# Optimization experiments

Hardware: AMD Instinct MI355X
Metric: run time of the kernel (lower is better)

The kernel has to match this reference:

```python
import jax, jax.numpy as jnp
import numpy as np

# ---- static radial-bin geometry (h == w == 512) ----
H = W = 512
_y, _x = np.indices((H, W))
_center = np.array([(_x.max() - _x.min()) / 2.0, (_y.max() - _y.min()) / 2.0])
_r = np.hypot(_x - _center[0], _y - _center[1])
_r_int = _r.astype(int)
NBINS = int(_r_int.max()) + 1            # all integer radii 0..NBINS-1 are present
R_INT = jnp.asarray(_r_int.ravel())       # (H*W,) int32 bin id per pixel
COUNTS = jnp.asarray(np.bincount(_r_int.ravel(), minlength=NBINS).astype(np.float32))

EPS = 1e-8


def _get_mask(freq_ri):
    """Vectorized equivalent of PSDLoss.get_mask. freq_ri: (n,c,h,w,2).

    azimuthalAverage's sort+cumsum binning == per-integer-radius mean,
    excluding bin 0 and the last bin. The sequential np.where idx-scan in
    psd1D_circle_mask is equivalent to a gather psd_ext[r_int] because psd
    values lie in [0,1] (the only possible collision, value 1.0 at idx=1,
    rewrites bin 0 with psd_ext[1] == psd_ext[0], a no-op).
    """
    comp = (freq_ri[..., 0] + EPS) + 1j * freq_ri[..., 1]   # freq_np += 1e-8
    mag = 20.0 * jnp.log(jnp.abs(comp))                      # magnitude spectrum
    n, c, h, w = mag.shape
    flat = mag.reshape(n, c, h * w)
    seg = lambda m: jax.ops.segment_sum(m, R_INT, num_segments=NBINS)
    sums = jax.vmap(jax.vmap(seg))(flat)                     # (n,c,NBINS)
    binmean = sums / COUNTS
    psd = binmean[..., 1:NBINS - 1]                          # bins 1..NBINS-2
    pmin = psd.min(axis=-1, keepdims=True)
    pmax = psd.max(axis=-1, keepdims=True)
    psd = (psd - pmin) / (pmax - pmin)                       # normalize to [0,1]
    # extend: prepend psd[0], append 0 -> length NBINS, indexed by r_int
    zero = jnp.zeros(psd.shape[:-1] + (1,), psd.dtype)
    psd_ext = jnp.concatenate([psd[..., :1], psd, zero], axis=-1)  # (n,c,NBINS)
    mask = jnp.take(psd_ext, R_INT, axis=-1).reshape(n, c, h, w)
    return mask


def _tensor2freq(img):
    f = jnp.fft.fftshift(jnp.fft.fft2(img), axes=(2, 3))
    return jnp.stack([f.real, f.imag], axis=-1)              # (n,c,h,w,2)


def reference(pred, target):
    loss_weight = 1.0
    pred_freq = _tensor2freq(pred)
    target_freq = _tensor2freq(target)
    # norm='l2', weight='recon', matrix=None (defaults)
    tmp = pred_freq ** 2 - target_freq ** 2
    tmp = tmp[..., 0] + tmp[..., 1]
    freq_distance = tmp ** 2
    mask_all = jax.lax.stop_gradient(_get_mask(pred_freq))   # detached weight
    wmat = 1.0 - mask_all
    wmat = jnp.where(jnp.isnan(wmat), 0.0, wmat)
    wmat = jnp.clip(wmat, 0.0, 1.0)
    return jnp.mean(wmat * freq_distance) * loss_weight


def setup_inputs() -> dict:
    key = jax.random.key(0)
    k1, k2 = jax.random.split(key)
    pred = jax.random.normal(k1, (8, 3, 512, 512), dtype=jnp.float32)
    target = jax.random.normal(k2, (8, 3, 512, 512), dtype=jnp.float32)
    return {"pred": pred, "target": target}
```

## Files before the change

### kernel.cpp

```cpp
#include <hip/hip_runtime.h>
#include <math.h>

#define HW 512
#define NIMG 24
#define NB 362
#define PLANE (HW*HW)
#define NC 257
#define NG 65
#define NPB (NIMG*NG)
#define CP2 133120

#define OFF_PM  0
#define OFF_PD  (NPB*NB)
#define OFF_PR  (2*NPB*NB)
#define OFF_PIm (OFF_PR + NIMG*CP2)
#define OFF_TR  (OFF_PR + 2*NIMG*CP2)
#define OFF_TI  (OFF_PR + 3*NIMG*CP2)
#define OFF_RM  (OFF_PR + 4*NIMG*CP2)
#define OFF_RD  (OFF_RM + NIMG*NB)

__device__ __forceinline__ int rbin_odd(float u, float v) {
    return (int)(sqrtf(fmaf(u, u, v*v)) * 0.5f);
}

__device__ __forceinline__ void cmul(float& xr, float& xi, float wr, float wi) {
    float r = xr*wr - xi*wi;
    xi = xr*wi + xi*wr;
    xr = r;
}

__device__ __forceinline__ void dft8(float ar[8], float ai[8]) {
    const float C = 0.70710678118654752440f;
    float t0r=ar[0]+ar[4], t0i=ai[0]+ai[4];
    float t1r=ar[0]-ar[4], t1i=ai[0]-ai[4];
    float t2r=ar[2]+ar[6], t2i=ai[2]+ai[6];
    float t3r=ar[2]-ar[6], t3i=ai[2]-ai[6];
    float E0r=t0r+t2r, E0i=t0i+t2i;
    float E2r=t0r-t2r, E2i=t0i-t2i;
    float E1r=t1r+t3i, E1i=t1i-t3r;
    float E3r=t1r-t3i, E3i=t1i+t3r;
    float u0r=ar[1]+ar[5], u0i=ai[1]+ai[5];
    float u1r=ar[1]-ar[5], u1i=ai[1]-ai[5];
    float u2r=ar[3]+ar[7], u2i=ai[3]+ai[7];
    float u3r=ar[3]-ar[7], u3i=ai[3]-ai[7];
    float O0r=u0r+u2r, O0i=u0i+u2i;
    float O2r=u0r-u2r, O2i=u0i-u2i;
    float O1r=u1r+u3i, O1i=u1i-u3r;
    float O3r=u1r-u3i, O3i=u1i+u3r;
    float W1r = C*(O1r+O1i), W1i = C*(O1i-O1r);
    float W2r = O2i,         W2i = -O2r;
    float W3r = C*(O3i-O3r), W3i = -C*(O3r+O3i);
    ar[0]=E0r+O0r; ai[0]=E0i+O0i;
    ar[4]=E0r-O0r; ai[4]=E0i-O0i;
    ar[1]=E1r+W1r; ai[1]=E1i+W1i;
    ar[5]=E1r-W1r; ai[5]=E1i-W1i;
    ar[2]=E2r+W2r; ai[2]=E2i+W2i;
    ar[6]=E2r-W2r; ai[6]=E2i-W2i;
    ar[3]=E3r+W3r; ai[3]=E3i+W3i;
    ar[7]=E3r-W3r; ai[7]=E3i-W3i;
}

__device__ __forceinline__ void twiddle7(float ar[8], float ai[8], float wr, float wi) {
    float pr = wr, pi = wi;
    cmul(ar[1], ai[1], pr, pi);
    #pragma unroll
    for (int k = 2; k < 8; ++k) {
        float nr = pr*wr - pi*wi;
        pi = pr*wi + pi*wr;
        pr = nr;
        cmul(ar[k], ai[k], pr, pi);
    }
}

__device__ __forceinline__ void fft512x2(float Ar[8], float Ai[8],
                                         float Br[8], float Bi[8],
                                         float* Lr, float* Li, int lane) {
    float s1, c1, s2, c2;
    int k1 = lane >> 3, b = lane & 7;
    __sincosf((float)lane * (-6.28318530717958647692f/512.0f), &s1, &c1);
    __sincosf((float)b    * (-6.28318530717958647692f/64.0f),  &s2, &c2);
    dft8(Ar, Ai); twiddle7(Ar, Ai, c1, s1);
    dft8(Br, Bi); twiddle7(Br, Bi, c1, s1);
    #pragma unroll
    for (int j = 0; j < 8; ++j) { Lr[j*68+lane] = Ar[j]; Li[j*68+lane] = Ai[j]; }
    #pragma unroll
    for (int a = 0; a < 8; ++a) { Ar[a] = Lr[k1*68+8*a+b]; Ai[a] = Li[k1*68+8*a+b]; }
    #pragma unroll
    for (int j = 0; j < 8; ++j) { Lr[j*68+lane] = Br[j]; Li[j*68+lane] = Bi[j]; }
    dft8(Ar, Ai); twiddle7(Ar, Ai, c2, s2);
    #pragma unroll
    for (int a = 0; a < 8; ++a) { Br[a] = Lr[k1*68+8*a+b]; Bi[a] = Li[k1*68+8*a+b]; }
    dft8(Br, Bi); twiddle7(Br, Bi, c2, s2);
    #pragma unroll
    for (int cc = 0; cc < 8; ++cc) {
        int ad = k1*68 + 8*cc + ((b + cc) & 7);
        Lr[ad] = Ar[cc]; Li[ad] = Ai[cc];
    }
    #pragma unroll
    for (int bb = 0; bb < 8; ++bb) {
        int ad = k1*68 + 8*b + ((bb + b) & 7);
        Ar[bb] = Lr[ad]; Ai[bb] = Li[ad];
    }
    #pragma unroll
    for (int cc = 0; cc < 8; ++cc) {
        int ad = k1*68 + 8*cc + ((b + cc) & 7);
        Lr[ad] = Br[cc]; Li[ad] = Bi[cc];
    }
    dft8(Ar, Ai);
    #pragma unroll
    for (int bb = 0; bb < 8; ++bb) {
        int ad = k1*68 + 8*b + ((bb + b) & 7);
        Br[bb] = Lr[ad]; Bi[bb] = Li[ad];
    }
    dft8(Br, Bi);
}

__global__ __launch_bounds__(256, 4) void k_rowfft(const float* __restrict__ pred,
                                                   const float* __restrict__ tgt,
                                                   float* __restrict__ ws) {
    __shared__ float smem[4352];
    int t = threadIdx.x, lane = t & 63, w = t >> 6;
    int b = blockIdx.x;
    int img = b >> 6;
    int r0 = (b & 63) << 3;
    int rA = r0 + 2*w;
    const float* pA = pred + (size_t)img*PLANE + (size_t)rA*HW;
    const float* tA = tgt  + (size_t)img*PLANE + (size_t)rA*HW;
    float arA[8], aiA[8], arB[8], aiB[8];
    #pragma unroll
    for (int j = 0; j < 8; ++j) {
        arA[j] = pA[64*j + lane];      aiA[j] = tA[64*j + lane];
        arB[j] = pA[HW + 64*j + lane]; aiB[j] = tA[HW + 64*j + lane];
    }
    float* Lr = smem + w*1088;
    float* Li = Lr + 544;
    fft512x2(arA, aiA, arB, aiB, Lr, Li, lane);
    float PrA[4], PiA[4], TrA[4], TiA[4], P256A=0.f, T256A=0.f;
    float PrB[4], PiB[4], TrB[4], TiB[4], P256B=0.f, T256B=0.f;
    #pragma unroll
    for (int d = 0; d < 8; ++d) {
        int k = (lane>>3) + ((lane&7)<<3) + (d<<6);
        Lr[k] = arA[d]; Li[k] = aiA[d];
    }
    #pragma unroll
    for (int m = 0; m < 4; ++m) {
        int kk = 64*m + lane, j2 = (512 - kk) & 511;
        float z1r = Lr[kk], z1i = Li[kk], z2r = Lr[j2], z2i = Li[j2];
        PrA[m] = 0.5f*(z1r+z2r); PiA[m] = 0.5f*(z1i-z2i);
        TrA[m] = 0.5f*(z1i+z2i); TiA[m] = 0.5f*(z2r-z1r);
    }
    if (lane == 0) { P256A = Lr[256]; T256A = Li[256]; }
    #pragma unroll
    for (int d = 0; d < 8; ++d) {
        int k = (lane>>3) + ((lane&7)<<3) + (d<<6);
        Lr[k] = arB[d]; Li[k] = aiB[d];
    }
    #pragma unroll
    for (int m = 0; m < 4; ++m) {
        int kk = 64*m + lane, j2 = (512 - kk) & 511;
        float z1r = Lr[kk], z1i = Li[kk], z2r = Lr[j2], z2i = Li[j2];
        PrB[m] = 0.5f*(z1r+z2r); PiB[m] = 0.5f*(z1i-z2i);
        TrB[m] = 0.5f*(z1i+z2i); TiB[m] = 0.5f*(z2r-z1r);
    }
    if (lane == 0) { P256B = Lr[256]; T256B = Li[256]; }

    float* tR = smem;
    float* tI = smem + 2080;
    __syncthreads();
    #pragma unroll
    for (int m = 0; m < 4; ++m) {
        int kk = 64*m + lane;
        tR[(2*w)*260 + kk]   = PrA[m]; tR[(2*w+1)*260 + kk] = PrB[m];
        tI[(2*w)*260 + kk]   = PiA[m]; tI[(2*w+1)*260 + kk] = PiB[m];
    }
    if (lane == 0) {
        tR[(2*w)*260 + 256] = P256A; tR[(2*w+1)*260 + 256] = P256B;
        tI[(2*w)*260 + 256] = 0.f;   tI[(2*w+1)*260 + 256] = 0.f;
    }
    __syncthreads();
    for (int idx = t; idx < 1040; idx += 256) {
        int comp = idx >= 520;
        int q = idx - (comp ? 520 : 0);
        int cg = q >> 3, rl = q & 7;
        const float* Tt = comp ? tI : tR;
        float4 v = *(const float4*)(Tt + rl*260 + 4*cg);
        float* outP = ws + (size_t)(comp ? OFF_PIm : OFF_PR)
                      + (size_t)img*CP2 + cg*2048 + (r0 + rl)*4;
        *(float4*)outP = v;
    }
    __syncthreads();
    #pragma unroll
    for (int m = 0; m < 4; ++m) {
        int kk = 64*m + lane;
        tR[(2*w)*260 + kk]   = TrA[m]; tR[(2*w+1)*260 + kk] = TrB[m];
        tI[(2*w)*260 + kk]   = TiA[m]; tI[(2*w+1)*260 + kk] = TiB[m];
    }
    if (lane == 0) {
        tR[(2*w)*260 + 256] = T256A; tR[(2*w+1)*260 + 256] = T256B;
        tI[(2*w)*260 + 256] = 0.f;   tI[(2*w+1)*260 + 256] = 0.f;
    }
    __syncthreads();
    for (int idx = t; idx < 1040; idx += 256) {
        int comp = idx >= 520;
        int q = idx - (comp ? 520 : 0);
        int cg = q >> 3, rl = q & 7;
        const float* Tt = comp ? tI : tR;
        float4 v = *(const float4*)(Tt + rl*260 + 4*cg);
        float* outP = ws + (size_t)(comp ? OFF_TI : OFF_TR)
                      + (size_t)img*CP2 + cg*2048 + (r0 + rl)*4;
        *(float4*)outP = v;
    }
}

__device__ __forceinline__ void flush2(float* binM, float* binD, int k,
                                       float aM, float aD) {
    atomicAdd(&binM[k], aM);
    atomicAdd(&binD[k], aD);
}

__global__ __launch_bounds__(256, 4) void k_colfft(const float* __restrict__ ws,
                                                   float* __restrict__ gPM,
                                                   float* __restrict__ gPD) {
    __shared__ float smem[4352];
    __shared__ float binM[NB], binD[NB];
    int t = threadIdx.x, lane = t & 63, w = t >> 6;
    for (int j = t; j < NB; j += 256) { binM[j] = 0.f; binD[j] = 0.f; }
    __syncthreads();
    int b = blockIdx.x;
    int img = b / NG;
    int g = b - img*NG;
    int c = 4*g + w;
    if (c < NC) {
        float* Lr = smem + w*1088;
        float* Li = Lr + 544;
        float prm[8], pim[8], trm[8], tim[8];
        size_t cbase = (size_t)img*CP2 + (size_t)(c >> 2)*2048 + (c & 3);
        const float* cPR = ws + OFF_PR  + cbase;
        const float* cPI = ws + OFF_PIm + cbase;
        const float* cTR = ws + OFF_TR  + cbase;
        const float* cTI = ws + OFF_TI  + cbase;
        #pragma unroll
        for (int j = 0; j < 8; ++j) {
            int o = (64*j + lane) << 2;
            prm[j] = cPR[o]; pim[j] = cPI[o];
            trm[j] = cTR[o]; tim[j] = cTI[o];
        }
        fft512x2(prm, pim, trm, tim, Lr, Li, lane);
        #pragma unroll
        for (int d = 0; d < 8; ++d) {
            int ky = (lane>>3) + ((lane&7)<<3) + (d<<6);
            float sp  = prm[d]*prm[d] + pim[d]*pim[d];
            float st_ = trm[d]*trm[d] + tim[d]*tim[d];
            float diff = sp - st_;
            float er = prm[d] + 1e-8f;
            Lr[ky] = 10.0f * __logf(er*er + pim[d]*pim[d]);
            Li[ky] = diff*diff;
        }
        __builtin_amdgcn_wave_barrier();
        int p0 = 4*lane;
        float4 fM = *(const float4*)(Lr + p0);
        float4 fD = *(const float4*)(Li + p0);
        float4 bM = *(const float4*)(Lr + 508 - p0);
        float4 bD = *(const float4*)(Li + 508 - p0);
        float eM = Lr[p0 + 4], eD = Li[p0 + 4];
        int gidx = (512 - p0) & 511;
        float gM = Lr[gidx], gD = Li[gidx];
        float sM[4], sD[4];
        sM[0]=fM.x+bM.w; sM[1]=fM.y+bM.z; sM[2]=fM.z+bM.y; sM[3]=fM.w+bM.x;
        sD[0]=fD.x+bD.w; sD[1]=fD.y+bD.z; sD[2]=fD.z+bD.y; sD[3]=fD.w+bD.x;
        float v1 = (c == 256) ? 511.0f : (float)(2*c + 1);
        {
            int kp = rbin_odd((float)(2*p0 + 1), v1);
            float aM = sM[0], aD = sD[0];
            #pragma unroll
            for (int j = 1; j < 4; ++j) {
                int k = rbin_odd((float)(2*(p0 + j) + 1), v1);
                if (k == kp) { aM += sM[j]; aD += sD[j]; }
                else { flush2(binM, binD, kp, aM, aD); kp = k; aM = sM[j]; aD = sD[j]; }
            }
            flush2(binM, binD, kp, aM, aD);
        }
        if (c >= 1 && c <= 255) {
            float s2M[4], s2D[4];
            s2M[0]=gM+fM.y;   s2D[0]=gD+fD.y;
            s2M[1]=bM.w+fM.z; s2D[1]=bD.w+fD.z;
            s2M[2]=bM.z+fM.w; s2D[2]=bD.z+fD.w;
            s2M[3]=bM.y+eM;   s2D[3]=bD.y+eD;
            float v2 = (float)(2*c - 1);
            int kp = rbin_odd((float)(2*p0 + 1), v2);
            float aM = s2M[0], aD = s2D[0];
            #pragma unroll
            for (int j = 1; j < 4; ++j) {
                int k = rbin_odd((float)(2*(p0 + j) + 1), v2);
                if (k == kp) { aM += s2M[j]; aD += s2D[j]; }
                else { flush2(binM, binD, kp, aM, aD); kp = k; aM = s2M[j]; aD = s2D[j]; }
            }
            flush2(binM, binD, kp, aM, aD);
        }
    }
    __syncthreads();
    for (int j = t; j < NB; j += 256) {
        gPM[(size_t)b*NB + j] = binM[j];
        gPD[(size_t)b*NB + j] = binD[j];
    }
}

__global__ __launch_bounds__(256) void k_reduce(const float* __restrict__ gPM,
                                                const float* __restrict__ gPD,
                                                float* __restrict__ rM,
                                                float* __restrict__ rD) {
    __shared__ float sm[8][33], sd2[8][33];
    int b = blockIdx.x;
    int img = b / 12, ch = b - img*12;
    int jl = threadIdx.x & 31, gs = threadIdx.x >> 5;
    int j = ch*32 + jl;
    float aM = 0.f, aD = 0.f;
    if (j < NB) {
        for (int g = gs; g < NG; g += 8) {
            aM += gPM[(size_t)(img*NG + g)*NB + j];
            aD += gPD[(size_t)(img*NG + g)*NB + j];
        }
    }
    sm[gs][jl] = aM; sd2[gs][jl] = aD;
    __syncthreads();
    if (threadIdx.x < 32 && j < NB) {
        float tM = 0.f, tD = 0.f;
        #pragma unroll
        for (int s = 0; s < 8; ++s) { tM += sm[s][jl]; tD += sd2[s][jl]; }
        rM[img*NB + j] = tM;
        rD[img*NB + j] = tD;
    }
}

__global__ __launch_bounds__(512) void k_final(const float* __restrict__ rM,
                                               const float* __restrict__ rD,
                                               float* __restrict__ out) {
    __shared__ int cnt[NB];
    __shared__ float meanb[NB];
    __shared__ float dsum[NB];
    __shared__ float rmin[512], rmax[512];
    __shared__ double sred[512];
    int t = threadIdx.x, img = blockIdx.x;
    for (int j = t; j < NB; j += 512) cnt[j] = 0;
    __syncthreads();
    {
        float u = (float)(2*(t >> 1) + 1);
        int vb = (t & 1) << 7;
        int kp = rbin_odd(u, (float)(2*vb + 1));
        int acc = 4;
        for (int i = 1; i < 128; ++i) {
            int k = rbin_odd(u, (float)(2*(vb + i) + 1));
            if (k == kp) acc += 4;
            else { atomicAdd(&cnt[kp], acc); kp = k; acc = 4; }
        }
        atomicAdd(&cnt[kp], acc);
    }
    __syncthreads();
    for (int j = t; j < NB; j += 512) {
        meanb[j] = rM[img*NB + j] / (float)cnt[j];
        dsum[j]  = rD[img*NB + j];
    }
    __syncthreads();
    float vmin = INFINITY, vmax = -INFINITY;
    if (t >= 1 && t <= 360) { vmin = meanb[t]; vmax = meanb[t]; }
    rmin[t] = vmin; rmax[t] = vmax;
    __syncthreads();
    for (int s = 256; s > 0; s >>= 1) {
        if (t < s) {
            float a = rmin[t], bb = rmin[t+s];
            rmin[t] = (a != a || bb != bb) ? __int_as_float(0x7fc00000) : fminf(a, bb);
            a = rmax[t]; bb = rmax[t+s];
            rmax[t] = (a != a || bb != bb) ? __int_as_float(0x7fc00000) : fmaxf(a, bb);
        }
        __syncthreads();
    }
    float pmin = rmin[0], pmax = rmax[0];
    double part = 0.0;
    for (int k = t; k < NB; k += 512) {
        float wgt;
        if (k == NB - 1) {
            wgt = 1.0f;
        } else {
            int idx = (k == 0) ? 1 : k;
            float e = (meanb[idx] - pmin) / (pmax - pmin);
            float wv = 1.0f - e;
            if (wv != wv) wv = 0.0f;
            wv = fminf(fmaxf(wv, 0.0f), 1.0f);
            wgt = wv;
        }
        part += (double)wgt * (double)dsum[k];
    }
    sred[t] = part;
    __syncthreads();
    for (int s = 256; s > 0; s >>= 1) {
        if (t < s) sred[t] += sred[t+s];
        __syncthreads();
    }
    if (t == 0) atomicAdd(out, (float)(sred[0] / 6291456.0));
}

extern "C" void kernel_launch(void* const* d_in, const int* in_sizes, int n_in,
                              void* d_out, int out_size, void* d_ws, size_t ws_size,
                              hipStream_t stream) {
    const float* pred = (const float*)d_in[0];
    const float* tgt  = (const float*)d_in[1];
    float* ws = (float*)d_ws;
    hipMemsetAsync(d_out, 0, sizeof(float), stream);
    k_rowfft<<<NIMG*64, 256, 0, stream>>>(pred, tgt, ws);
    k_colfft<<<NPB, 256, 0, stream>>>(ws, ws + OFF_PM, ws + OFF_PD);
    k_reduce<<<NIMG*12, 256, 0, stream>>>(ws + OFF_PM, ws + OFF_PD,
                                          ws + OFF_RM, ws + OFF_RD);
    k_final<<<NIMG, 512, 0, stream>>>(ws + OFF_RM, ws + OFF_RD, (float*)d_out);
}
```

Baseline: 155.8 us.

## Reorder row-FFT intermediate layout so column FFT loads contiguous float4 pairs

Each row-FFT block now handles rows strided by 64 (qb, qb+64, ...) instead of 8 consecutive rows, and writes its per-column results as 8 contiguous floats at col*512 + qb*8. That places the elements each column-FFT lane needs, rows lane+64*j, next to each other, so the column kernel reads them with two float4 loads per array instead of eight strided scalar loads. The intermediate buffer shrinks to 257*512 per image. In exchange, the shared-memory transpose reads become scalar and strided, and the global writes are 32-byte chunks spread across columns.

```diff
diff --git a/kernel.cpp b/kernel.cpp
--- a/kernel.cpp
+++ b/kernel.cpp
@@ -8,15 +8,16 @@
 #define NC 257
 #define NG 65
 #define NPB (NIMG*NG)
-#define CP2 133120
+#define CPC 131584
+
 
 #define OFF_PM  0
 #define OFF_PD  (NPB*NB)
 #define OFF_PR  (2*NPB*NB)
-#define OFF_PIm (OFF_PR + NIMG*CP2)
-#define OFF_TR  (OFF_PR + 2*NIMG*CP2)
-#define OFF_TI  (OFF_PR + 3*NIMG*CP2)
-#define OFF_RM  (OFF_PR + 4*NIMG*CP2)
+#define OFF_PIm (OFF_PR + NIMG*CPC)
+#define OFF_TR  (OFF_PR + 2*NIMG*CPC)
+#define OFF_TI  (OFF_PR + 3*NIMG*CPC)
+#define OFF_RM  (OFF_PR + 4*NIMG*CPC)
 #define OFF_RD  (OFF_RM + NIMG*NB)
 
 __device__ __forceinline__ int rbin_odd(float u, float v) {
@@ -122,15 +123,15 @@
     int t = threadIdx.x, lane = t & 63, w = t >> 6;
     int b = blockIdx.x;
     int img = b >> 6;
-    int r0 = (b & 63) << 3;
-    int rA = r0 + 2*w;
+    int qb = b & 63;
+    int rA = 128*w + qb;
     const float* pA = pred + (size_t)img*PLANE + (size_t)rA*HW;
     const float* tA = tgt  + (size_t)img*PLANE + (size_t)rA*HW;
     float arA[8], aiA[8], arB[8], aiB[8];
     #pragma unroll
     for (int j = 0; j < 8; ++j) {
-        arA[j] = pA[64*j + lane];      aiA[j] = tA[64*j + lane];
-        arB[j] = pA[HW + 64*j + lane]; aiB[j] = tA[HW + 64*j + lane];
+        arA[j] = pA[64*j + lane];         aiA[j] = tA[64*j + lane];
+        arB[j] = pA[64*HW + 64*j + lane]; aiB[j] = tA[64*HW + 64*j + lane];
     }
     float* Lr = smem + w*1088;
     float* Li = Lr + 544;
@@ -178,15 +179,19 @@
         tI[(2*w)*260 + 256] = 0.f;   tI[(2*w+1)*260 + 256] = 0.f;
     }
     __syncthreads();
-    for (int idx = t; idx < 1040; idx += 256) {
-        int comp = idx >= 520;
-        int q = idx - (comp ? 520 : 0);
-        int cg = q >> 3, rl = q & 7;
+    for (int idx = t; idx < 514; idx += 256) {
+        int comp = idx >= 257;
+        int col = comp ? (idx - 257) : idx;
         const float* Tt = comp ? tI : tR;
-        float4 v = *(const float4*)(Tt + rl*260 + 4*cg);
+        float4 v0, v1;
+        v0.x = Tt[        col]; v0.y = Tt[ 260 + col];
+        v0.z = Tt[ 520 + col];  v0.w = Tt[ 780 + col];
+        v1.x = Tt[1040 + col];  v1.y = Tt[1300 + col];
+        v1.z = Tt[1560 + col];  v1.w = Tt[1820 + col];
         float* outP = ws + (size_t)(comp ? OFF_PIm : OFF_PR)
-                      + (size_t)img*CP2 + cg*2048 + (r0 + rl)*4;
-        *(float4*)outP = v;
+                      + (size_t)img*CPC + (size_t)col*512 + qb*8;
+        *(float4*)outP = v0;
+        *(float4*)(outP + 4) = v1;
     }
     __syncthreads();
     #pragma unroll
@@ -200,15 +205,19 @@
         tI[(2*w)*260 + 256] = 0.f;   tI[(2*w+1)*260 + 256] = 0.f;
     }
     __syncthreads();
-    for (int idx = t; idx < 1040; idx += 256) {
-        int comp = idx >= 520;
-        int q = idx - (comp ? 520 : 0);
-        int cg = q >> 3, rl = q & 7;
+    for (int idx = t; idx < 514; idx += 256) {
+        int comp = idx >= 257;
+        int col = comp ? (idx - 257) : idx;
         const float* Tt = comp ? tI : tR;
-        float4 v = *(const float4*)(Tt + rl*260 + 4*cg);
+        float4 v0, v1;
+        v0.x = Tt[        col]; v0.y = Tt[ 260 + col];
+        v0.z = Tt[ 520 + col];  v0.w = Tt[ 780 + col];
+        v1.x = Tt[1040 + col];  v1.y = Tt[1300 + col];
+        v1.z = Tt[1560 + col];  v1.w = Tt[1820 + col];
         float* outP = ws + (size_t)(comp ? OFF_TI : OFF_TR)
-                      + (size_t)img*CP2 + cg*2048 + (r0 + rl)*4;
-        *(float4*)outP = v;
+                      + (size_t)img*CPC + (size_t)col*512 + qb*8;
+        *(float4*)outP = v0;
+        *(float4*)(outP + 4) = v1;
     }
 }
 
@@ -233,18 +242,19 @@
     if (c < NC) {
         float* Lr = smem + w*1088;
         float* Li = Lr + 544;
-        float prm[8], pim[8], trm[8], tim[8];
-        size_t cbase = (size_t)img*CP2 + (size_t)(c >> 2)*2048 + (c & 3);
-        const float* cPR = ws + OFF_PR  + cbase;
-        const float* cPI = ws + OFF_PIm + cbase;
-        const float* cTR = ws + OFF_TR  + cbase;
-        const float* cTI = ws + OFF_TI  + cbase;
-        #pragma unroll
-        for (int j = 0; j < 8; ++j) {
-            int o = (64*j + lane) << 2;
-            prm[j] = cPR[o]; pim[j] = cPI[o];
-            trm[j] = cTR[o]; tim[j] = cTI[o];
-        }
+        size_t cb = (size_t)img*CPC + (size_t)c*512 + (size_t)(lane*8);
+        const float* cPR = ws + OFF_PR  + cb;
+        const float* cPI = ws + OFF_PIm + cb;
+        const float* cTR = ws + OFF_TR  + cb;
+        const float* cTI = ws + OFF_TI  + cb;
+        float4 pr0 = *(const float4*)cPR, pr1 = *(const float4*)(cPR + 4);
+        float4 pi0 = *(const float4*)cPI, pi1 = *(const float4*)(cPI + 4);
+        float4 tr0 = *(const float4*)cTR, tr1 = *(const float4*)(cTR + 4);
+        float4 ti0 = *(const float4*)cTI, ti1 = *(const float4*)(cTI + 4);
+        float prm[8] = {pr0.x,pr0.y,pr0.z,pr0.w,pr1.x,pr1.y,pr1.z,pr1.w};
+        float pim[8] = {pi0.x,pi0.y,pi0.z,pi0.w,pi1.x,pi1.y,pi1.z,pi1.w};
+        float trm[8] = {tr0.x,tr0.y,tr0.z,tr0.w,tr1.x,tr1.y,tr1.z,tr1.w};
+        float tim[8] = {ti0.x,ti0.y,ti0.z,ti0.w,ti1.x,ti1.y,ti1.z,ti1.w};
         fft512x2(prm, pim, trm, tim, Lr, Li, lane);
         #pragma unroll
         for (int d = 0; d < 8; ++d) {
```

New measurement: 167.8 us. 7.7% more time.

## Process two columns per wave in column FFT and halve block count

Applied to the files above, without the earlier changes.

The column-FFT kernel now has each wave transform two complex columns at once (four real signals: pred and target for each), using a new four-way FFT that interleaves the two columns' radix-8 stages through float2 shared memory. The grid shrinks to about half as many blocks, which halves the per-block partial bin arrays and the work in the reduce kernel. This aims to raise instruction-level parallelism per wave and cut block overhead and partial-sum traffic. In exchange it doubles register pressure per thread under launch_bounds(256,4), which can cause spills or lower occupancy, and the shared-memory footprint doubles.

```diff
diff --git a/kernel.cpp b/kernel.cpp
--- a/kernel.cpp
+++ b/kernel.cpp
@@ -6,13 +6,13 @@
 #define NB 362
 #define PLANE (HW*HW)
 #define NC 257
-#define NG 65
-#define NPB (NIMG*NG)
+#define NG2 33
+#define NPB2 (NIMG*NG2)
 #define CP2 133120
 
 #define OFF_PM  0
-#define OFF_PD  (NPB*NB)
-#define OFF_PR  (2*NPB*NB)
+#define OFF_PD  (NPB2*NB)
+#define OFF_PR  (2*NPB2*NB)
 #define OFF_PIm (OFF_PR + NIMG*CP2)
 #define OFF_TR  (OFF_PR + 2*NIMG*CP2)
 #define OFF_TI  (OFF_PR + 3*NIMG*CP2)
@@ -115,6 +115,84 @@
     dft8(Br, Bi);
 }
 
+__device__ __forceinline__ void fft512x4(
+        float Ar[8], float Ai[8], float Br[8], float Bi[8],
+        float Cr[8], float Ci[8], float Dr[8], float Di[8],
+        float2* L1, float2* L2, int lane) {
+    float s1, c1, s2, c2;
+    int k1 = lane >> 3, b = lane & 7;
+    __sincosf((float)lane * (-6.28318530717958647692f/512.0f), &s1, &c1);
+    __sincosf((float)b    * (-6.28318530717958647692f/64.0f),  &s2, &c2);
+    dft8(Ar, Ai); twiddle7(Ar, Ai, c1, s1);
+    dft8(Br, Bi); twiddle7(Br, Bi, c1, s1);
+    dft8(Cr, Ci); twiddle7(Cr, Ci, c1, s1);
+    dft8(Dr, Di); twiddle7(Dr, Di, c1, s1);
+    #pragma unroll
+    for (int j = 0; j < 8; ++j) L1[j*68+lane] = make_float2(Ar[j], Ai[j]);
+    #pragma unroll
+    for (int j = 0; j < 8; ++j) L2[j*68+lane] = make_float2(Cr[j], Ci[j]);
+    #pragma unroll
+    for (int a = 0; a < 8; ++a) { float2 v = L1[k1*68+8*a+b]; Ar[a]=v.x; Ai[a]=v.y; }
+    #pragma unroll
+    for (int a = 0; a < 8; ++a) { float2 v = L2[k1*68+8*a+b]; Cr[a]=v.x; Ci[a]=v.y; }
+    #pragma unroll
+    for (int j = 0; j < 8; ++j) L1[j*68+lane] = make_float2(Br[j], Bi[j]);
+    #pragma unroll
+    for (int j = 0; j < 8; ++j) L2[j*68+lane] = make_float2(Dr[j], Di[j]);
+    dft8(Ar, Ai); twiddle7(Ar, Ai, c2, s2);
+    dft8(Cr, Ci); twiddle7(Cr, Ci, c2, s2);
+    #pragma unroll
+    for (int a = 0; a < 8; ++a) { float2 v = L1[k1*68+8*a+b]; Br[a]=v.x; Bi[a]=v.y; }
+    #pragma unroll
+    for (int a = 0; a < 8; ++a) { float2 v = L2[k1*68+8*a+b]; Dr[a]=v.x; Di[a]=v.y; }
+    dft8(Br, Bi); twiddle7(Br, Bi, c2, s2);
+    dft8(Dr, Di); twiddle7(Dr, Di, c2, s2);
+    #pragma unroll
+    for (int cc = 0; cc < 8; ++cc) {
+        int ad = k1*68 + 8*cc + ((b + cc) & 7);
+        L1[ad] = make_float2(Ar[cc], Ai[cc]);
+    }
+    #pragma unroll
+    for (int cc = 0; cc < 8; ++cc) {
+        int ad = k1*68 + 8*cc + ((b + cc) & 7);
+        L2[ad] = make_float2(Cr[cc], Ci[cc]);
+    }
+    #pragma unroll
+    for (int bb = 0; bb < 8; ++bb) {
+        int ad = k1*68 + 8*b + ((bb + b) & 7);
+        float2 v = L1[ad]; Ar[bb] = v.x; Ai[bb] = v.y;
+    }
+    #pragma unroll
+    for (int bb = 0; bb < 8; ++bb) {
+        int ad = k1*68 + 8*b + ((bb + b) & 7);
+        float2 v = L2[ad]; Cr[bb] = v.x; Ci[bb] = v.y;
+    }
+    #pragma unroll
+    for (int cc = 0; cc < 8; ++cc) {
+        int ad = k1*68 + 8*cc + ((b + cc) & 7);
+        L1[ad] = make_float2(Br[cc], Bi[cc]);
+    }
+    #pragma unroll
+    for (int cc = 0; cc < 8; ++cc) {
+        int ad = k1*68 + 8*cc + ((b + cc) & 7);
+        L2[ad] = make_float2(Dr[cc], Di[cc]);
+    }
+    dft8(Ar, Ai);
+    dft8(Cr, Ci);
+    #pragma unroll
+    for (int bb = 0; bb < 8; ++bb) {
+        int ad = k1*68 + 8*b + ((bb + b) & 7);
+        float2 v = L1[ad]; Br[bb] = v.x; Bi[bb] = v.y;
+    }
+    #pragma unroll
+    for (int bb = 0; bb < 8; ++bb) {
+        int ad = k1*68 + 8*b + ((bb + b) & 7);
+        float2 v = L2[ad]; Dr[bb] = v.x; Di[bb] = v.y;
+    }
+    dft8(Br, Bi);
+    dft8(Dr, Di);
+}
+
 __global__ __launch_bounds__(256, 4) void k_rowfft(const float* __restrict__ pred,
                                                    const float* __restrict__ tgt,
                                                    float* __restrict__ ws) {
@@ -218,85 +296,104 @@
     atomicAdd(&binD[k], aD);
 }
 
+__device__ __forceinline__ void bin_column(const float2* LC, int c, int lane,
+                                           float* binM, float* binD) {
+    int p0 = 4*lane;
+    float4 q0  = *(const float4*)(LC + p0);
+    float4 q1  = *(const float4*)(LC + p0 + 2);
+    float4 r0v = *(const float4*)(LC + (508 - p0));
+    float4 r1v = *(const float4*)(LC + (510 - p0));
+    float2 e2 = LC[p0 + 4];
+    float2 g2 = LC[(512 - p0) & 511];
+    float sM[4], sD[4];
+    sM[0]=q0.x+r1v.z; sM[1]=q0.z+r1v.x; sM[2]=q1.x+r0v.z; sM[3]=q1.z+r0v.x;
+    sD[0]=q0.y+r1v.w; sD[1]=q0.w+r1v.y; sD[2]=q1.y+r0v.w; sD[3]=q1.w+r0v.y;
+    float v1 = (c == 256) ? 511.0f : (float)(2*c + 1);
+    {
+        int kp = rbin_odd((float)(2*p0 + 1), v1);
+        float aM = sM[0], aD = sD[0];
+        #pragma unroll
+        for (int j = 1; j < 4; ++j) {
+            int k = rbin_odd((float)(2*(p0 + j) + 1), v1);
+            if (k == kp) { aM += sM[j]; aD += sD[j]; }
+            else { flush2(binM, binD, kp, aM, aD); kp = k; aM = sM[j]; aD = sD[j]; }
+        }
+        flush2(binM, binD, kp, aM, aD);
+    }
+    if (c >= 1 && c <= 255) {
+        float s2M[4], s2D[4];
+        s2M[0]=g2.x+q0.z;   s2D[0]=g2.y+q0.w;
+        s2M[1]=r1v.z+q1.x;  s2D[1]=r1v.w+q1.y;
+        s2M[2]=r1v.x+q1.z;  s2D[2]=r1v.y+q1.w;
+        s2M[3]=r0v.z+e2.x;  s2D[3]=r0v.w+e2.y;
+        float v2 = (float)(2*c - 1);
+        int kp = rbin_odd((float)(2*p0 + 1), v2);
+        float aM = s2M[0], aD = s2D[0];
+        #pragma unroll
+        for (int j = 1; j < 4; ++j) {
+            int k = rbin_odd((float)(2*(p0 + j) + 1), v2);
+            if (k == kp) { aM += s2M[j]; aD += s2D[j]; }
+            else { flush2(binM, binD, kp, aM, aD); kp = k; aM = s2M[j]; aD = s2D[j]; }
+        }
+        flush2(binM, binD, kp, aM, aD);
+    }
+}
+
 __global__ __launch_bounds__(256, 4) void k_colfft(const float* __restrict__ ws,
                                                    float* __restrict__ gPM,
                                                    float* __restrict__ gPD) {
-    __shared__ float smem[4352];
+    __shared__ __align__(16) float2 smem2[4352];
     __shared__ float binM[NB], binD[NB];
     int t = threadIdx.x, lane = t & 63, w = t >> 6;
     for (int j = t; j < NB; j += 256) { binM[j] = 0.f; binD[j] = 0.f; }
     __syncthreads();
     int b = blockIdx.x;
-    int img = b / NG;
-    int g = b - img*NG;
-    int c = 4*g + w;
-    if (c < NC) {
-        float* Lr = smem + w*1088;
-        float* Li = Lr + 544;
-        float prm[8], pim[8], trm[8], tim[8];
-        size_t cbase = (size_t)img*CP2 + (size_t)(c >> 2)*2048 + (c & 3);
-        const float* cPR = ws + OFF_PR  + cbase;
-        const float* cPI = ws + OFF_PIm + cbase;
-        const float* cTR = ws + OFF_TR  + cbase;
-        const float* cTI = ws + OFF_TI  + cbase;
+    int img = b / NG2;
+    int g = b - img*NG2;
+    int cA = 8*g + w;
+    int cB = cA + 4;
+    bool doA = (cA < NC), doB = (cB < NC);
+    if (doA) {
+        float2* L1 = smem2 + w*1088;
+        float2* L2 = L1 + 544;
+        float pr1[8], pi1[8], tr1[8], ti1[8];
+        float pr2[8], pi2[8], tr2[8], ti2[8];
+        size_t cbA = (size_t)img*CP2 + (size_t)(cA >> 2)*2048 + (cA & 3);
+        size_t cbB = doB ? (cbA + 2048) : cbA;
+        const float* aPR = ws + OFF_PR  + cbA;
+        const float* aPI = ws + OFF_PIm + cbA;
+        const float* aTR = ws + OFF_TR  + cbA;
+        const float* aTI = ws + OFF_TI  + cbA;
+        const float* bPR = ws + OFF_PR  + cbB;
+        const float* bPI = ws + OFF_PIm + cbB;
+        const float* bTR = ws + OFF_TR  + cbB;
+        const float* bTI = ws + OFF_TI  + cbB;
         #pragma unroll
         for (int j = 0; j < 8; ++j) {
             int o = (64*j + lane) << 2;
-            prm[j] = cPR[o]; pim[j] = cPI[o];
-            trm[j] = cTR[o]; tim[j] = cTI[o];
-        }
-        fft512x2(prm, pim, trm, tim, Lr, Li, lane);
+            pr1[j] = aPR[o]; pi1[j] = aPI[o];
+            tr1[j] = aTR[o]; ti1[j] = aTI[o];
+            pr2[j] = bPR[o]; pi2[j] = bPI[o];
+            tr2[j] = bTR[o]; ti2[j] = bTI[o];
+        }
+        fft512x4(pr1, pi1, tr1, ti1, pr2, pi2, tr2, ti2, L1, L2, lane);
         #pragma unroll
         for (int d = 0; d < 8; ++d) {
             int ky = (lane>>3) + ((lane&7)<<3) + (d<<6);
-            float sp  = prm[d]*prm[d] + pim[d]*pim[d];
-            float st_ = trm[d]*trm[d] + tim[d]*tim[d];
-            float diff = sp - st_;
-            float er = prm[d] + 1e-8f;
-            Lr[ky] = 10.0f * __logf(er*er + pim[d]*pim[d]);
-            Li[ky] = diff*diff;
+            float spA = pr1[d]*pr1[d] + pi1[d]*pi1[d];
+            float stA = tr1[d]*tr1[d] + ti1[d]*ti1[d];
+            float dfA = spA - stA;
+            float erA = pr1[d] + 1e-8f;
+            L1[ky] = make_float2(10.0f * __logf(erA*erA + pi1[d]*pi1[d]), dfA*dfA);
+            float spB = pr2[d]*pr2[d] + pi2[d]*pi2[d];
+            float stB = tr2[d]*tr2[d] + ti2[d]*ti2[d];
+            float dfB = spB - stB;
+            float erB = pr2[d] + 1e-8f;
+            L2[ky] = make_float2(10.0f * __logf(erB*erB + pi2[d]*pi2[d]), dfB*dfB);
         }
         __builtin_amdgcn_wave_barrier();
-        int p0 = 4*lane;
-        float4 fM = *(const float4*)(Lr + p0);
-        float4 fD = *(const float4*)(Li + p0);
-        float4 bM = *(const float4*)(Lr + 508 - p0);
-        float4 bD = *(const float4*)(Li + 508 - p0);
-        float eM = Lr[p0 + 4], eD = Li[p0 + 4];
-        int gidx = (512 - p0) & 511;
-        float gM = Lr[gidx], gD = Li[gidx];
-        float sM[4], sD[4];
-        sM[0]=fM.x+bM.w; sM[1]=fM.y+bM.z; sM[2]=fM.z+bM.y; sM[3]=fM.w+bM.x;
-        sD[0]=fD.x+bD.w; sD[1]=fD.y+bD.z; sD[2]=fD.z+bD.y; sD[3]=fD.w+bD.x;
-        float v1 = (c == 256) ? 511.0f : (float)(2*c + 1);
-        {
-            int kp = rbin_odd((float)(2*p0 + 1), v1);
-            float aM = sM[0], aD = sD[0];
-            #pragma unroll
-            for (int j = 1; j < 4; ++j) {
-                int k = rbin_odd((float)(2*(p0 + j) + 1), v1);
-                if (k == kp) { aM += sM[j]; aD += sD[j]; }
-                else { flush2(binM, binD, kp, aM, aD); kp = k; aM = sM[j]; aD = sD[j]; }
-            }
-            flush2(binM, binD, kp, aM, aD);
-        }
-        if (c >= 1 && c <= 255) {
-            float s2M[4], s2D[4];
-            s2M[0]=gM+fM.y;   s2D[0]=gD+fD.y;
-            s2M[1]=bM.w+fM.z; s2D[1]=bD.w+fD.z;
-            s2M[2]=bM.z+fM.w; s2D[2]=bD.z+fD.w;
-            s2M[3]=bM.y+eM;   s2D[3]=bD.y+eD;
-            float v2 = (float)(2*c - 1);
-            int kp = rbin_odd((float)(2*p0 + 1), v2);
-            float aM = s2M[0], aD = s2D[0];
-            #pragma unroll
-            for (int j = 1; j < 4; ++j) {
-                int k = rbin_odd((float)(2*(p0 + j) + 1), v2);
-                if (k == kp) { aM += s2M[j]; aD += s2D[j]; }
-                else { flush2(binM, binD, kp, aM, aD); kp = k; aM = s2M[j]; aD = s2D[j]; }
-            }
-            flush2(binM, binD, kp, aM, aD);
-        }
+        bin_column(L1, cA, lane, binM, binD);
+        if (doB) bin_column(L2, cB, lane, binM, binD);
     }
     __syncthreads();
     for (int j = t; j < NB; j += 256) {
@@ -316,9 +413,9 @@
     int j = ch*32 + jl;
     float aM = 0.f, aD = 0.f;
     if (j < NB) {
-        for (int g = gs; g < NG; g += 8) {
-            aM += gPM[(size_t)(img*NG + g)*NB + j];
-            aD += gPD[(size_t)(img*NG + g)*NB + j];
+        for (int g = gs; g < NG2; g += 8) {
+            aM += gPM[(size_t)(img*NG2 + g)*NB + j];
+            aD += gPD[(size_t)(img*NG2 + g)*NB + j];
         }
     }
     sm[gs][jl] = aM; sd2[gs][jl] = aD;
@@ -407,7 +504,7 @@
     float* ws = (float*)d_ws;
     hipMemsetAsync(d_out, 0, sizeof(float), stream);
     k_rowfft<<<NIMG*64, 256, 0, stream>>>(pred, tgt, ws);
-    k_colfft<<<NPB, 256, 0, stream>>>(ws, ws + OFF_PM, ws + OFF_PD);
+    k_colfft<<<NPB2, 256, 0, stream>>>(ws, ws + OFF_PM, ws + OFF_PD);
     k_reduce<<<NIMG*12, 256, 0, stream>>>(ws + OFF_PM, ws + OFF_PD,
                                           ws + OFF_RM, ws + OFF_RD);
     k_final<<<NIMG, 512, 0, stream>>>(ws + OFF_RM, ws + OFF_RD, (float*)d_out);
```

Measured after the change: 162.1 us. +4.0%, slower.

## Split column FFT of pred and target across separate waves per column

Applied to the files above, without the earlier changes.

The column-FFT kernel now uses 512 threads per block, so each column gets two waves: one transforms the pred spectrum and the other the target spectrum, each with a single-signal FFT in interleaved float2 LDS. The waves exchange magnitude and power results through shared memory after a block barrier. Binning also splits by role: one wave handles the primary mirror pairing and the other the secondary pairing. The aim is more parallelism and lower per-thread register pressure. The cost is a block-wide sync and more LDS traffic per column.

```diff
diff --git a/kernel.cpp b/kernel.cpp
--- a/kernel.cpp
+++ b/kernel.cpp
@@ -115,6 +115,31 @@
     dft8(Br, Bi);
 }
 
+__device__ __forceinline__ void fft512x1(float Ar[8], float Ai[8],
+                                         float2* L, int lane) {
+    float s1, c1, s2, c2;
+    int k1 = lane >> 3, b = lane & 7;
+    __sincosf((float)lane * (-6.28318530717958647692f/512.0f), &s1, &c1);
+    __sincosf((float)b    * (-6.28318530717958647692f/64.0f),  &s2, &c2);
+    dft8(Ar, Ai); twiddle7(Ar, Ai, c1, s1);
+    #pragma unroll
+    for (int j = 0; j < 8; ++j) L[j*68+lane] = make_float2(Ar[j], Ai[j]);
+    #pragma unroll
+    for (int a = 0; a < 8; ++a) { float2 v = L[k1*68+8*a+b]; Ar[a]=v.x; Ai[a]=v.y; }
+    dft8(Ar, Ai); twiddle7(Ar, Ai, c2, s2);
+    #pragma unroll
+    for (int cc = 0; cc < 8; ++cc) {
+        int ad = k1*68 + 8*cc + ((b + cc) & 7);
+        L[ad] = make_float2(Ar[cc], Ai[cc]);
+    }
+    #pragma unroll
+    for (int bb = 0; bb < 8; ++bb) {
+        int ad = k1*68 + 8*b + ((bb + b) & 7);
+        float2 v = L[ad]; Ar[bb] = v.x; Ai[bb] = v.y;
+    }
+    dft8(Ar, Ai);
+}
+
 __global__ __launch_bounds__(256, 4) void k_rowfft(const float* __restrict__ pred,
                                                    const float* __restrict__ tgt,
                                                    float* __restrict__ ws) {
@@ -218,58 +243,72 @@
     atomicAdd(&binD[k], aD);
 }
 
-__global__ __launch_bounds__(256, 4) void k_colfft(const float* __restrict__ ws,
+__global__ __launch_bounds__(512, 4) void k_colfft(const float* __restrict__ ws,
                                                    float* __restrict__ gPM,
                                                    float* __restrict__ gPD) {
-    __shared__ float smem[4352];
+    __shared__ __align__(16) float2 scr[8*544];
     __shared__ float binM[NB], binD[NB];
     int t = threadIdx.x, lane = t & 63, w = t >> 6;
-    for (int j = t; j < NB; j += 256) { binM[j] = 0.f; binD[j] = 0.f; }
+    for (int j = t; j < NB; j += 512) { binM[j] = 0.f; binD[j] = 0.f; }
     __syncthreads();
     int b = blockIdx.x;
     int img = b / NG;
     int g = b - img*NG;
-    int c = 4*g + w;
+    int c = 4*g + (w >> 1);
+    int role = w & 1;
+    float2* L = scr + w*544;
     if (c < NC) {
-        float* Lr = smem + w*1088;
-        float* Li = Lr + 544;
-        float prm[8], pim[8], trm[8], tim[8];
+        float re[8], im[8];
         size_t cbase = (size_t)img*CP2 + (size_t)(c >> 2)*2048 + (c & 3);
-        const float* cPR = ws + OFF_PR  + cbase;
-        const float* cPI = ws + OFF_PIm + cbase;
-        const float* cTR = ws + OFF_TR  + cbase;
-        const float* cTI = ws + OFF_TI  + cbase;
+        const float* bre = ws + (role ? OFF_TR : OFF_PR)  + cbase;
+        const float* bim = ws + (role ? OFF_TI : OFF_PIm) + cbase;
         #pragma unroll
         for (int j = 0; j < 8; ++j) {
             int o = (64*j + lane) << 2;
-            prm[j] = cPR[o]; pim[j] = cPI[o];
-            trm[j] = cTR[o]; tim[j] = cTI[o];
-        }
-        fft512x2(prm, pim, trm, tim, Lr, Li, lane);
-        #pragma unroll
-        for (int d = 0; d < 8; ++d) {
-            int ky = (lane>>3) + ((lane&7)<<3) + (d<<6);
-            float sp  = prm[d]*prm[d] + pim[d]*pim[d];
-            float st_ = trm[d]*trm[d] + tim[d]*tim[d];
-            float diff = sp - st_;
-            float er = prm[d] + 1e-8f;
-            Lr[ky] = 10.0f * __logf(er*er + pim[d]*pim[d]);
-            Li[ky] = diff*diff;
-        }
-        __builtin_amdgcn_wave_barrier();
+            re[j] = bre[o]; im[j] = bim[o];
+        }
+        fft512x1(re, im, L, lane);
+        if (role == 0) {
+            #pragma unroll
+            for (int d = 0; d < 8; ++d) {
+                int ky = (lane>>3) + ((lane&7)<<3) + (d<<6);
+                float sp = re[d]*re[d] + im[d]*im[d];
+                float er = re[d] + 1e-8f;
+                L[ky] = make_float2(10.0f * __logf(er*er + im[d]*im[d]), sp);
+            }
+        } else {
+            float* Lf = (float*)L;
+            #pragma unroll
+            for (int d = 0; d < 8; ++d) {
+                int ky = (lane>>3) + ((lane&7)<<3) + (d<<6);
+                Lf[ky] = re[d]*re[d] + im[d]*im[d];
+            }
+        }
+    }
+    __syncthreads();
+    if (c < NC) {
+        const float2* LP = scr + (size_t)(w & ~1)*544;
+        const float*  LT = (const float*)(scr + (size_t)((w & ~1) + 1)*544);
         int p0 = 4*lane;
-        float4 fM = *(const float4*)(Lr + p0);
-        float4 fD = *(const float4*)(Li + p0);
-        float4 bM = *(const float4*)(Lr + 508 - p0);
-        float4 bD = *(const float4*)(Li + 508 - p0);
-        float eM = Lr[p0 + 4], eD = Li[p0 + 4];
-        int gidx = (512 - p0) & 511;
-        float gM = Lr[gidx], gD = Li[gidx];
-        float sM[4], sD[4];
-        sM[0]=fM.x+bM.w; sM[1]=fM.y+bM.z; sM[2]=fM.z+bM.y; sM[3]=fM.w+bM.x;
-        sD[0]=fD.x+bD.w; sD[1]=fD.y+bD.z; sD[2]=fD.z+bD.y; sD[3]=fD.w+bD.x;
-        float v1 = (c == 256) ? 511.0f : (float)(2*c + 1);
-        {
+        float4 a0 = *(const float4*)(LP + p0);
+        float4 a1 = *(const float4*)(LP + p0 + 2);
+        float4 tf = *(const float4*)(LT + p0);
+        float fM[4], fD[4];
+        fM[0]=a0.x; fM[1]=a0.z; fM[2]=a1.x; fM[3]=a1.z;
+        { float d0=a0.y-tf.x, d1=a0.w-tf.y, d2=a1.y-tf.z, d3=a1.w-tf.w;
+          fD[0]=d0*d0; fD[1]=d1*d1; fD[2]=d2*d2; fD[3]=d3*d3; }
+        float4 b0 = *(const float4*)(LP + (508 - p0));
+        float4 b1 = *(const float4*)(LP + (510 - p0));
+        float4 tb = *(const float4*)(LT + (508 - p0));
+        float bM[4], bD[4];
+        bM[0]=b0.x; bM[1]=b0.z; bM[2]=b1.x; bM[3]=b1.z;
+        { float d0=b0.y-tb.x, d1=b0.w-tb.y, d2=b1.y-tb.z, d3=b1.w-tb.w;
+          bD[0]=d0*d0; bD[1]=d1*d1; bD[2]=d2*d2; bD[3]=d3*d3; }
+        if (role == 0) {
+            float sM[4], sD[4];
+            #pragma unroll
+            for (int j = 0; j < 4; ++j) { sM[j] = fM[j] + bM[3-j]; sD[j] = fD[j] + bD[3-j]; }
+            float v1 = (c == 256) ? 511.0f : (float)(2*c + 1);
             int kp = rbin_odd((float)(2*p0 + 1), v1);
             float aM = sM[0], aD = sD[0];
             #pragma unroll
@@ -279,13 +318,16 @@
                 else { flush2(binM, binD, kp, aM, aD); kp = k; aM = sM[j]; aD = sD[j]; }
             }
             flush2(binM, binD, kp, aM, aD);
-        }
-        if (c >= 1 && c <= 255) {
+        } else if (c >= 1 && c <= 255) {
+            float2 ge = LP[(512 - p0) & 511]; float gt = LT[(512 - p0) & 511];
+            float gM_ = ge.x, gd = ge.y - gt; float gD_ = gd*gd;
+            float2 ee = LP[p0 + 4];           float et = LT[p0 + 4];
+            float eM_ = ee.x, ed = ee.y - et; float eD_ = ed*ed;
             float s2M[4], s2D[4];
-            s2M[0]=gM+fM.y;   s2D[0]=gD+fD.y;
-            s2M[1]=bM.w+fM.z; s2D[1]=bD.w+fD.z;
-            s2M[2]=bM.z+fM.w; s2D[2]=bD.z+fD.w;
-            s2M[3]=bM.y+eM;   s2D[3]=bD.y+eD;
+            s2M[0]=gM_  +fM[1]; s2D[0]=gD_  +fD[1];
+            s2M[1]=bM[3]+fM[2]; s2D[1]=bD[3]+fD[2];
+            s2M[2]=bM[2]+fM[3]; s2D[2]=bD[2]+fD[3];
+            s2M[3]=bM[1]+eM_;   s2D[3]=bD[1]+eD_;
             float v2 = (float)(2*c - 1);
             int kp = rbin_odd((float)(2*p0 + 1), v2);
             float aM = s2M[0], aD = s2D[0];
@@ -299,7 +341,7 @@
         }
     }
     __syncthreads();
-    for (int j = t; j < NB; j += 256) {
+    for (int j = t; j < NB; j += 512) {
         gPM[(size_t)b*NB + j] = binM[j];
         gPD[(size_t)b*NB + j] = binD[j];
     }
@@ -407,7 +449,7 @@
     float* ws = (float*)d_ws;
     hipMemsetAsync(d_out, 0, sizeof(float), stream);
     k_rowfft<<<NIMG*64, 256, 0, stream>>>(pred, tgt, ws);
-    k_colfft<<<NPB, 256, 0, stream>>>(ws, ws + OFF_PM, ws + OFF_PD);
+    k_colfft<<<NPB, 512, 0, stream>>>(ws, ws + OFF_PM, ws + OFF_PD);
     k_reduce<<<NIMG*12, 256, 0, stream>>>(ws + OFF_PM, ws + OFF_PD,
                                           ws + OFF_RM, ws + OFF_RD);
     k_final<<<NIMG, 512, 0, stream>>>(ws + OFF_RM, ws + OFF_RD, (float*)d_out);
```

Result: no change. 155.3 us (-0.3%).
